# Kernel tuning notes

Hardware: AMD Instinct MI355X
Metric: run time of the kernel (lower is better)

Reference implementation:

```python
import jax, jax.numpy as jnp
import numpy as np

N_NODES = 50000
N_EDGES = 800000
D = 64  # node/edge/transformed feature size


def setup_inputs() -> dict:
    key = jax.random.key(0)
    ks = jax.random.split(key, 10)
    nodes = jax.random.normal(ks[0], (N_NODES, D), dtype=jnp.float32)
    edges = jax.random.normal(ks[1], (N_EDGES, D), dtype=jnp.float32)
    senders = jax.random.randint(ks[2], (N_EDGES,), 0, N_NODES, dtype=jnp.int32)
    receivers = jax.random.randint(ks[3], (N_EDGES,), 0, N_NODES, dtype=jnp.int32)
    # eqx.nn.Linear params: W [out, in], b [out]
    agg_edge_in = D + 2 * D       # edge + sender + receiver
    agg_node_in = D + 2 * D       # node + outgoing agg + incoming agg
    attn_in = 2 * D               # sender + receiver
    s = lambda fan_in: 1.0 / np.sqrt(fan_in)
    We = jax.random.uniform(ks[4], (D, agg_edge_in), jnp.float32, -s(agg_edge_in), s(agg_edge_in))
    be = jax.random.uniform(ks[5], (D,), jnp.float32, -s(agg_edge_in), s(agg_edge_in))
    Wn = jax.random.uniform(ks[6], (D, agg_node_in), jnp.float32, -s(agg_node_in), s(agg_node_in))
    bn = jax.random.uniform(ks[7], (D,), jnp.float32, -s(agg_node_in), s(agg_node_in))
    Wa = jax.random.uniform(ks[8], (1, attn_in), jnp.float32, -s(attn_in), s(attn_in))
    ba = jax.random.uniform(ks[9], (1,), jnp.float32, -s(attn_in), s(attn_in))
    return {"nodes": nodes, "edges": edges, "senders": senders, "receivers": receivers,
            "We": We, "be": be, "Wn": Wn, "bn": bn, "Wa": Wa, "ba": ba}


def reference(nodes, edges, senders, receivers, We, be, Wn, bn, Wa, ba):
    n = nodes.shape[0]
    sent = nodes[senders]      # [E, D] sender node features
    recv = nodes[receivers]    # [E, D] receiver node features

    # 1) update_edge_fn: concat + Linear + ReLU
    agg_e = jnp.concatenate((edges, sent, recv), axis=-1)          # [E, 3D]
    new_edges = jax.nn.relu(jnp.einsum('ei,oi->eo', agg_e, We) + be)

    # 2) attention_logit_fn: Linear on concat(sender, receiver)
    logits = jnp.einsum('ei,oi->eo', jnp.concatenate((sent, recv), axis=-1), Wa) + ba  # [E, 1]

    # 3) jraph segment_softmax over receivers (normalize per receiving node)
    seg_max = jax.ops.segment_max(logits, receivers, num_segments=n)
    ex = jnp.exp(logits - seg_max[receivers])
    denom = jax.ops.segment_sum(ex, receivers, num_segments=n)
    att = ex / denom[receivers]                                    # [E, 1]

    # attention_reduce_fn: elementwise weighting
    w_edges = new_edges * att                                      # [E, D]

    # aggregate edges for nodes (jraph default: segment_sum)
    out_agg = jax.ops.segment_sum(w_edges, senders, num_segments=n)    # outgoing
    in_agg = jax.ops.segment_sum(w_edges, receivers, num_segments=n)   # incoming

    # 4) update_node_fn: concat + Linear + ReLU
    agg_n = jnp.concatenate((nodes, out_agg, in_agg), axis=-1)     # [N, 3D]
    new_nodes = jax.nn.relu(jnp.einsum('ni,oi->no', agg_n, Wn) + bn)
    return new_nodes, w_edges
```

## Files before the change

### kernel.cpp

```cpp
#include <hip/hip_runtime.h>

#define D 64

typedef __attribute__((ext_vector_type(8))) short bf16x8;
typedef __attribute__((ext_vector_type(4))) float f32x4;

static __device__ __forceinline__ unsigned short f2bf(float x) {
    union { float f; unsigned int u; } v; v.f = x;
    const unsigned int r = (v.u + 0x7fffu + ((v.u >> 16) & 1u)) >> 16;
    return (unsigned short)r;
}
static __device__ __forceinline__ float bf2f(unsigned short u) {
    union { unsigned int i; float f; } v; v.i = ((unsigned int)u) << 16; return v.f;
}

__global__ __launch_bounds__(256)
void premix_kernel(const float* __restrict__ nodes, const float* __restrict__ We,
                   const float* __restrict__ Wa,
                   unsigned short* __restrict__ PSb, unsigned short* __restrict__ PRb,
                   float* __restrict__ ps, float* __restrict__ pr, int N)
{
    __shared__ float sWS[64][68];
    __shared__ float sWR[64][68];
    __shared__ float sX[64][68];
    __shared__ float sWa[128];

    const int t = threadIdx.x;
    const int o = t & 63;
    const int k0 = (t >> 6) * 16;
#pragma unroll
    for (int k = 0; k < 16; ++k) {
        sWS[k0 + k][o] = We[(size_t)o * 192 + 64 + k0 + k];
        sWR[k0 + k][o] = We[(size_t)o * 192 + 128 + k0 + k];
    }
    if (t < 128) sWa[t] = Wa[t];

    const int nb = blockIdx.x * 64;
    const int ln = t & 63;
    const int gn = min(nb + ln, N - 1);
    {
        const float* src = nodes + (size_t)gn * D + k0;
        const f32x4 x0 = *(const f32x4*)(src + 0);
        const f32x4 x1 = *(const f32x4*)(src + 4);
        const f32x4 x2 = *(const f32x4*)(src + 8);
        const f32x4 x3 = *(const f32x4*)(src + 12);
        sX[k0 + 0][ln] = x0.x;  sX[k0 + 1][ln] = x0.y;
        sX[k0 + 2][ln] = x0.z;  sX[k0 + 3][ln] = x0.w;
        sX[k0 + 4][ln] = x1.x;  sX[k0 + 5][ln] = x1.y;
        sX[k0 + 6][ln] = x1.z;  sX[k0 + 7][ln] = x1.w;
        sX[k0 + 8][ln] = x2.x;  sX[k0 + 9][ln] = x2.y;
        sX[k0 + 10][ln] = x2.z; sX[k0 + 11][ln] = x2.w;
        sX[k0 + 12][ln] = x3.x; sX[k0 + 13][ln] = x3.y;
        sX[k0 + 14][ln] = x3.z; sX[k0 + 15][ln] = x3.w;
    }
    __syncthreads();

    const int o0 = (t & 15) * 4;
    const int rc = (t >> 4) * 4;
    float as[4][4] = {{0.f,0.f,0.f,0.f},{0.f,0.f,0.f,0.f},{0.f,0.f,0.f,0.f},{0.f,0.f,0.f,0.f}};
    float ar[4][4] = {{0.f,0.f,0.f,0.f},{0.f,0.f,0.f,0.f},{0.f,0.f,0.f,0.f},{0.f,0.f,0.f,0.f}};

#pragma unroll 8
    for (int ci = 0; ci < 64; ++ci) {
        const f32x4 xv = *(const f32x4*)&sX[ci][rc];
        const f32x4 ws = *(const f32x4*)&sWS[ci][o0];
        const f32x4 wr = *(const f32x4*)&sWR[ci][o0];
        as[0][0] += xv.x * ws.x; as[0][1] += xv.x * ws.y; as[0][2] += xv.x * ws.z; as[0][3] += xv.x * ws.w;
        as[1][0] += xv.y * ws.x; as[1][1] += xv.y * ws.y; as[1][2] += xv.y * ws.z; as[1][3] += xv.y * ws.w;
        as[2][0] += xv.z * ws.x; as[2][1] += xv.z * ws.y; as[2][2] += xv.z * ws.z; as[2][3] += xv.z * ws.w;
        as[3][0] += xv.w * ws.x; as[3][1] += xv.w * ws.y; as[3][2] += xv.w * ws.z; as[3][3] += xv.w * ws.w;
        ar[0][0] += xv.x * wr.x; ar[0][1] += xv.x * wr.y; ar[0][2] += xv.x * wr.z; ar[0][3] += xv.x * wr.w;
        ar[1][0] += xv.y * wr.x; ar[1][1] += xv.y * wr.y; ar[1][2] += xv.y * wr.z; ar[1][3] += xv.y * wr.w;
        ar[2][0] += xv.z * wr.x; ar[2][1] += xv.z * wr.y; ar[2][2] += xv.z * wr.z; ar[2][3] += xv.z * wr.w;
        ar[3][0] += xv.w * wr.x; ar[3][1] += xv.w * wr.y; ar[3][2] += xv.w * wr.z; ar[3][3] += xv.w * wr.w;
    }

#pragma unroll
    for (int j = 0; j < 4; ++j) {
        const int n = nb + rc + j;
        if (n < N) {
            ushort4 vs, vr;
            vs.x = f2bf(as[j][0]); vs.y = f2bf(as[j][1]); vs.z = f2bf(as[j][2]); vs.w = f2bf(as[j][3]);
            vr.x = f2bf(ar[j][0]); vr.y = f2bf(ar[j][1]); vr.z = f2bf(ar[j][2]); vr.w = f2bf(ar[j][3]);
            *(ushort4*)&PSb[(size_t)n * D + o0] = vs;
            *(ushort4*)&PRb[(size_t)n * D + o0] = vr;
        }
    }

    if (t < 64 && nb + t < N) {
        float p1 = 0.f, p2 = 0.f;
#pragma unroll 8
        for (int k = 0; k < 64; ++k) {
            const float x = sX[k][t];
            p1 += x * sWa[k];
            p2 += x * sWa[64 + k];
        }
        ps[nb + t] = p1;
        pr[nb + t] = p2;
    }
}

__global__ __launch_bounds__(256)
void edge_logit_kernel(const int* __restrict__ snd, const int* __restrict__ rcv,
                       const float* __restrict__ ps, const float* __restrict__ pr,
                       const float* __restrict__ ba, float* __restrict__ elog,
                       float* __restrict__ denom, int* __restrict__ deg_out,
                       int* __restrict__ deg_in, int E)
{
    const float bav = ba[0];
    const int stride = gridDim.x * blockDim.x;
    for (int e = blockIdx.x * blockDim.x + threadIdx.x; e < E; e += stride) {
        const int s = snd[e], r = rcv[e];
        const float ex = __expf(ps[s] + pr[r] + bav);
        elog[e] = ex;
        atomicAdd(&denom[r], ex);
        atomicAdd(&deg_out[s], 1);
        atomicAdd(&deg_in[r], 1);
    }
}

__global__ __launch_bounds__(1024)
void scan_kernel(const int* __restrict__ deg_out, int* __restrict__ off_out,
                 const int* __restrict__ deg_in, int* __restrict__ off_in, int N)
{
    const int* deg = (blockIdx.x == 0) ? deg_out : deg_in;
    int* off       = (blockIdx.x == 0) ? off_out : off_in;
    __shared__ int part[1024];
    const int t = threadIdx.x;
    const int CH = (((N + 1023) / 1024) + 3) & ~3;
    const int c0 = t * CH;
    int s = 0;
    if (c0 + CH <= N) {
#pragma unroll 4
        for (int k = 0; k < CH; k += 4) {
            const int4 v = *(const int4*)&deg[c0 + k];
            s += v.x + v.y + v.z + v.w;
        }
    } else {
        for (int k = 0; k < CH; ++k) {
            const int i = c0 + k;
            if (i < N) s += deg[i];
        }
    }
    part[t] = s;
    __syncthreads();
    for (int d = 1; d < 1024; d <<= 1) {
        int v = 0;
        if (t >= d) v = part[t - d];
        __syncthreads();
        part[t] += v;
        __syncthreads();
    }
    int run = (t == 0) ? 0 : part[t - 1];
    if (c0 + CH <= N) {
#pragma unroll 4
        for (int k = 0; k < CH; k += 4) {
            const int4 v = *(const int4*)&deg[c0 + k];
            int4 w;
            w.x = run; w.y = run + v.x; w.z = w.y + v.y; w.w = w.z + v.z;
            *(int4*)&off[c0 + k] = w;
            run = w.w + v.w;
        }
    } else {
        for (int k = 0; k < CH; ++k) {
            const int i = c0 + k;
            if (i < N) { off[i] = run; run += deg[i]; }
        }
    }
    if (t == 1023) off[N] = part[1023];
}

__global__ __launch_bounds__(256)
void edge_mix_kernel(const float* __restrict__ edges, const int* __restrict__ snd,
                     const int* __restrict__ rcv, const float* __restrict__ We,
                     const float* __restrict__ be,
                     const unsigned short* __restrict__ PSb,
                     const unsigned short* __restrict__ PRb,
                     const float* __restrict__ elog, const float* __restrict__ denom,
                     const int* __restrict__ off_out, const int* __restrict__ off_in,
                     int* __restrict__ cur_out, int* __restrict__ cur_in,
                     int* __restrict__ idx_out, int* __restrict__ idx_in,
                     float* __restrict__ w_out, int E)
{
    __shared__ unsigned short sX[64][72];
    __shared__ unsigned short sW[64][72];

    const int t = threadIdx.x;
    const int eb = blockIdx.x * 64;

    if (t < 128) {
        const int e = eb + (t & 63);
        if (e < E) {
            if (t < 64) {
                const int s = snd[e];
                const int po = atomicAdd(&cur_out[s], 1);
                idx_out[off_out[s] + po] = e;
            } else {
                const int r = rcv[e];
                const int pi = atomicAdd(&cur_in[r], 1);
                idx_in[off_in[r] + pi] = e;
            }
        }
    }

    {
        const int le = t & 63;
        const int k0 = (t >> 6) * 16;
        const int ge = min(eb + le, E - 1);
        const float* xsrc = edges + (size_t)ge * D + k0;
        const float* wsrc = We + (size_t)le * 192 + k0;
        const f32x4 x0 = *(const f32x4*)(xsrc + 0);
        const f32x4 x1 = *(const f32x4*)(xsrc + 4);
        const f32x4 x2 = *(const f32x4*)(xsrc + 8);
        const f32x4 x3 = *(const f32x4*)(xsrc + 12);
        const f32x4 w0 = *(const f32x4*)(wsrc + 0);
        const f32x4 w1 = *(const f32x4*)(wsrc + 4);
        const f32x4 w2 = *(const f32x4*)(wsrc + 8);
        const f32x4 w3 = *(const f32x4*)(wsrc + 12);
        uint4 xp, wp;
        xp.x = (unsigned)f2bf(x0.x) | ((unsigned)f2bf(x0.y) << 16);
        xp.y = (unsigned)f2bf(x0.z) | ((unsigned)f2bf(x0.w) << 16);
        xp.z = (unsigned)f2bf(x1.x) | ((unsigned)f2bf(x1.y) << 16);
        xp.w = (unsigned)f2bf(x1.z) | ((unsigned)f2bf(x1.w) << 16);
        *(uint4*)&sX[le][k0] = xp;
        xp.x = (unsigned)f2bf(x2.x) | ((unsigned)f2bf(x2.y) << 16);
        xp.y = (unsigned)f2bf(x2.z) | ((unsigned)f2bf(x2.w) << 16);
        xp.z = (unsigned)f2bf(x3.x) | ((unsigned)f2bf(x3.y) << 16);
        xp.w = (unsigned)f2bf(x3.z) | ((unsigned)f2bf(x3.w) << 16);
        *(uint4*)&sX[le][k0 + 8] = xp;
        wp.x = (unsigned)f2bf(w0.x) | ((unsigned)f2bf(w0.y) << 16);
        wp.y = (unsigned)f2bf(w0.z) | ((unsigned)f2bf(w0.w) << 16);
        wp.z = (unsigned)f2bf(w1.x) | ((unsigned)f2bf(w1.y) << 16);
        wp.w = (unsigned)f2bf(w1.z) | ((unsigned)f2bf(w1.w) << 16);
        *(uint4*)&sW[le][k0] = wp;
        wp.x = (unsigned)f2bf(w2.x) | ((unsigned)f2bf(w2.y) << 16);
        wp.y = (unsigned)f2bf(w2.z) | ((unsigned)f2bf(w2.w) << 16);
        wp.z = (unsigned)f2bf(w3.x) | ((unsigned)f2bf(w3.y) << 16);
        wp.w = (unsigned)f2bf(w3.z) | ((unsigned)f2bf(w3.w) << 16);
        *(uint4*)&sW[le][k0 + 8] = wp;
    }
    __syncthreads();

    const int w   = t >> 6;
    const int l   = t & 63;
    const int r16 = l & 15;
    const int kb  = l >> 4;

    f32x4 acc[4] = {{0.f,0.f,0.f,0.f},{0.f,0.f,0.f,0.f},{0.f,0.f,0.f,0.f},{0.f,0.f,0.f,0.f}};
    const int er = w * 16 + r16;

#pragma unroll
    for (int kt = 0; kt < 2; ++kt) {
        const int kof = kt * 32 + kb * 8;
        const bf16x8 x = *(const bf16x8*)&sX[er][kof];
#pragma unroll
        for (int n = 0; n < 4; ++n) {
            const bf16x8 wv = *(const bf16x8*)&sW[n * 16 + r16][kof];
            acc[n] = __builtin_amdgcn_mfma_f32_16x16x32_bf16(wv, x, acc[n], 0, 0, 0);
        }
    }

    const int e = eb + er;
    if (e < E) {
        const int s = snd[e];
        const int r = rcv[e];
        const float att = elog[e] / denom[r];
        const int o0 = kb * 4;
        const unsigned short* psr = PSb + (size_t)s * D + o0;
        const unsigned short* prr = PRb + (size_t)r * D + o0;
        float* wo = w_out + (size_t)e * D + o0;
#pragma unroll
        for (int n = 0; n < 4; ++n) {
            const ushort4 psv = *(const ushort4*)(psr + n * 16);
            const ushort4 prv = *(const ushort4*)(prr + n * 16);
            const f32x4 bev = *(const f32x4*)&be[n * 16 + o0];
            f32x4 wv;
            wv.x = fmaxf(acc[n][0] + bf2f(psv.x) + bf2f(prv.x) + bev.x, 0.f) * att;
            wv.y = fmaxf(acc[n][1] + bf2f(psv.y) + bf2f(prv.y) + bev.y, 0.f) * att;
            wv.z = fmaxf(acc[n][2] + bf2f(psv.z) + bf2f(prv.z) + bev.z, 0.f) * att;
            wv.w = fmaxf(acc[n][3] + bf2f(psv.w) + bf2f(prv.w) + bev.w, 0.f) * att;
            *(f32x4*)(wo + n * 16) = wv;
        }
    }
}

__global__ __launch_bounds__(256)
void agg_kernel(const float* __restrict__ w_edges,
                const int* __restrict__ idx_out, const int* __restrict__ off_out,
                const int* __restrict__ idx_in, const int* __restrict__ off_in,
                float* __restrict__ out_agg, float* __restrict__ in_agg, int N)
{
    const int lane = threadIdx.x & 63;
    const int wid  = (blockIdx.x * blockDim.x + threadIdx.x) >> 6;
    if (wid >= 2 * N) return;
    const bool is_out = wid < N;
    const int node = is_out ? wid : wid - N;
    const int* __restrict__ idx = is_out ? idx_out : idx_in;
    const int* __restrict__ off = is_out ? off_out : off_in;
    float* __restrict__ dst = is_out ? out_agg : in_agg;

    const int a = off[node], b = off[node + 1];
    float acc = 0.f;
    int j = a;
    for (; j + 3 < b; j += 4) {
        const int e0 = idx[j], e1 = idx[j + 1], e2 = idx[j + 2], e3 = idx[j + 3];
        const float v0 = w_edges[(size_t)e0 * D + lane];
        const float v1 = w_edges[(size_t)e1 * D + lane];
        const float v2 = w_edges[(size_t)e2 * D + lane];
        const float v3 = w_edges[(size_t)e3 * D + lane];
        acc += v0 + v1 + v2 + v3;
    }
    for (; j < b; ++j) acc += w_edges[(size_t)idx[j] * D + lane];
    dst[(size_t)node * D + lane] = acc;
}

__global__ __launch_bounds__(256)
void node_out_kernel(const float* __restrict__ nodes, const float* __restrict__ oag,
                     const float* __restrict__ iag, const float* __restrict__ Wn,
                     const float* __restrict__ bn, float* __restrict__ out, int N)
{
    __shared__ float sW[64][68];
    __shared__ float sX[64][68];

    const int t = threadIdx.x;
    const int o = t & 63;
    const int k0 = (t >> 6) * 16;
    const int nb = blockIdx.x * 64;
    const int ln = t & 63;
    const int gn = min(nb + ln, N - 1);
    const int o0 = (t & 15) * 4;
    const int rc = (t >> 4) * 4;

    float acc[4][4] = {{0.f,0.f,0.f,0.f},{0.f,0.f,0.f,0.f},{0.f,0.f,0.f,0.f},{0.f,0.f,0.f,0.f}};

#pragma unroll
    for (int g = 0; g < 3; ++g) {
        const float* xbase = (g == 0) ? nodes : ((g == 1) ? oag : iag);
        const float* src = xbase + (size_t)gn * D + k0;
        const f32x4 x0 = *(const f32x4*)(src + 0);
        const f32x4 x1 = *(const f32x4*)(src + 4);
        const f32x4 x2 = *(const f32x4*)(src + 8);
        const f32x4 x3 = *(const f32x4*)(src + 12);
        __syncthreads();
#pragma unroll
        for (int k = 0; k < 16; ++k) {
            sW[k0 + k][o] = Wn[(size_t)o * 192 + g * 64 + k0 + k];
        }
        sX[k0 + 0][ln] = x0.x;  sX[k0 + 1][ln] = x0.y;
        sX[k0 + 2][ln] = x0.z;  sX[k0 + 3][ln] = x0.w;
        sX[k0 + 4][ln] = x1.x;  sX[k0 + 5][ln] = x1.y;
        sX[k0 + 6][ln] = x1.z;  sX[k0 + 7][ln] = x1.w;
        sX[k0 + 8][ln] = x2.x;  sX[k0 + 9][ln] = x2.y;
        sX[k0 + 10][ln] = x2.z; sX[k0 + 11][ln] = x2.w;
        sX[k0 + 12][ln] = x3.x; sX[k0 + 13][ln] = x3.y;
        sX[k0 + 14][ln] = x3.z; sX[k0 + 15][ln] = x3.w;
        __syncthreads();
#pragma unroll 8
        for (int ci = 0; ci < 64; ++ci) {
            const f32x4 xv = *(const f32x4*)&sX[ci][rc];
            const f32x4 wv = *(const f32x4*)&sW[ci][o0];
            acc[0][0] += xv.x * wv.x; acc[0][1] += xv.x * wv.y; acc[0][2] += xv.x * wv.z; acc[0][3] += xv.x * wv.w;
            acc[1][0] += xv.y * wv.x; acc[1][1] += xv.y * wv.y; acc[1][2] += xv.y * wv.z; acc[1][3] += xv.y * wv.w;
            acc[2][0] += xv.z * wv.x; acc[2][1] += xv.z * wv.y; acc[2][2] += xv.z * wv.z; acc[2][3] += xv.z * wv.w;
            acc[3][0] += xv.w * wv.x; acc[3][1] += xv.w * wv.y; acc[3][2] += xv.w * wv.z; acc[3][3] += xv.w * wv.w;
        }
    }

    const f32x4 bnv = *(const f32x4*)&bn[o0];
#pragma unroll
    for (int j = 0; j < 4; ++j) {
        const int n = nb + rc + j;
        if (n < N) {
            f32x4 y;
            y.x = fmaxf(acc[j][0] + bnv.x, 0.f);
            y.y = fmaxf(acc[j][1] + bnv.y, 0.f);
            y.z = fmaxf(acc[j][2] + bnv.z, 0.f);
            y.w = fmaxf(acc[j][3] + bnv.w, 0.f);
            *(f32x4*)&out[(size_t)n * D + o0] = y;
        }
    }
}

extern "C" void kernel_launch(void* const* d_in, const int* in_sizes, int n_in,
                              void* d_out, int out_size, void* d_ws, size_t ws_size,
                              hipStream_t stream) {
    const float* nodes = (const float*)d_in[0];
    const float* edges = (const float*)d_in[1];
    const int*   snd   = (const int*)d_in[2];
    const int*   rcv   = (const int*)d_in[3];
    const float* We    = (const float*)d_in[4];
    const float* be    = (const float*)d_in[5];
    const float* Wn    = (const float*)d_in[6];
    const float* bn    = (const float*)d_in[7];
    const float* Wa    = (const float*)d_in[8];
    const float* ba    = (const float*)d_in[9];

    const int N = in_sizes[0] / D;
    const int E = in_sizes[2];

    float* out_nodes = (float*)d_out;
    float* w_out     = (float*)d_out + (size_t)N * D;

    char* w = (char*)d_ws;
    float* denom   = (float*)w;                 w += (size_t)N * 4;
    int*   deg_out = (int*)w;                   w += (size_t)N * 4;
    int*   deg_in  = (int*)w;                   w += (size_t)N * 4;
    int*   cur_out = (int*)w;                   w += (size_t)N * 4;
    int*   cur_in  = (int*)w;                   w += (size_t)N * 4;
    float* ps      = (float*)w;                 w += (size_t)N * 4;
    float* pr      = (float*)w;                 w += (size_t)N * 4;
    int*   off_out = (int*)w;                   w += (size_t)(N + 1) * 4;
    int*   off_in  = (int*)w;                   w += (size_t)(N + 1) * 4;
    float* elog    = (float*)w;                 w += (size_t)E * 4;
    int*   idx_out = (int*)w;                   w += (size_t)E * 4;
    int*   idx_in  = (int*)w;                   w += (size_t)E * 4;
    unsigned short* PSb = (unsigned short*)w;   w += (size_t)N * D * 2;
    unsigned short* PRb = (unsigned short*)w;   w += (size_t)N * D * 2;
    float* out_agg = (float*)w;                 w += (size_t)N * D * 4;
    float* in_agg  = (float*)w;

    hipMemsetAsync(denom, 0, (size_t)5 * N * 4, stream);

    premix_kernel<<<(N + 63) / 64, 256, 0, stream>>>(nodes, We, Wa, PSb, PRb, ps, pr, N);

    edge_logit_kernel<<<1024, 256, 0, stream>>>(snd, rcv, ps, pr, ba, elog,
                                                denom, deg_out, deg_in, E);

    scan_kernel<<<2, 1024, 0, stream>>>(deg_out, off_out, deg_in, off_in, N);

    edge_mix_kernel<<<(E + 63) / 64, 256, 0, stream>>>(edges, snd, rcv, We, be,
                                                       PSb, PRb, elog, denom,
                                                       off_out, off_in, cur_out, cur_in,
                                                       idx_out, idx_in, w_out, E);

    agg_kernel<<<(2 * N + 3) / 4, 256, 0, stream>>>(w_out, idx_out, off_out,
                                                    idx_in, off_in, out_agg, in_agg, N);

    node_out_kernel<<<(N + 63) / 64, 256, 0, stream>>>(nodes, out_agg, in_agg,
                                                       Wn, bn, out_nodes, N);
}
```

Baseline: 503.1 us.

## Make edge_mix persistent with register-resident weights and direct MFMA operand loads

```diff
diff --git a/kernel.cpp b/kernel.cpp
--- a/kernel.cpp
+++ b/kernel.cpp
@@ -12,6 +12,14 @@
 }
 static __device__ __forceinline__ float bf2f(unsigned short u) {
     union { unsigned int i; float f; } v; v.i = ((unsigned int)u) << 16; return v.f;
+}
+static __device__ __forceinline__ bf16x8 pack8(const f32x4 a, const f32x4 b) {
+    union { bf16x8 v; unsigned int u[4]; } p;
+    p.u[0] = (unsigned)f2bf(a.x) | ((unsigned)f2bf(a.y) << 16);
+    p.u[1] = (unsigned)f2bf(a.z) | ((unsigned)f2bf(a.w) << 16);
+    p.u[2] = (unsigned)f2bf(b.x) | ((unsigned)f2bf(b.y) << 16);
+    p.u[3] = (unsigned)f2bf(b.z) | ((unsigned)f2bf(b.w) << 16);
+    return p.v;
 }
 
 __global__ __launch_bounds__(256)
@@ -182,104 +190,71 @@
                      int* __restrict__ idx_out, int* __restrict__ idx_in,
                      float* __restrict__ w_out, int E)
 {
-    __shared__ unsigned short sX[64][72];
-    __shared__ unsigned short sW[64][72];
-
-    const int t = threadIdx.x;
-    const int eb = blockIdx.x * 64;
-
-    if (t < 128) {
-        const int e = eb + (t & 63);
-        if (e < E) {
-            if (t < 64) {
-                const int s = snd[e];
-                const int po = atomicAdd(&cur_out[s], 1);
-                idx_out[off_out[s] + po] = e;
-            } else {
-                const int r = rcv[e];
-                const int pi = atomicAdd(&cur_in[r], 1);
-                idx_in[off_in[r] + pi] = e;
-            }
-        }
-    }
-
-    {
-        const int le = t & 63;
-        const int k0 = (t >> 6) * 16;
-        const int ge = min(eb + le, E - 1);
-        const float* xsrc = edges + (size_t)ge * D + k0;
-        const float* wsrc = We + (size_t)le * 192 + k0;
-        const f32x4 x0 = *(const f32x4*)(xsrc + 0);
-        const f32x4 x1 = *(const f32x4*)(xsrc + 4);
-        const f32x4 x2 = *(const f32x4*)(xsrc + 8);
-        const f32x4 x3 = *(const f32x4*)(xsrc + 12);
-        const f32x4 w0 = *(const f32x4*)(wsrc + 0);
-        const f32x4 w1 = *(const f32x4*)(wsrc + 4);
-        const f32x4 w2 = *(const f32x4*)(wsrc + 8);
-        const f32x4 w3 = *(const f32x4*)(wsrc + 12);
-        uint4 xp, wp;
-        xp.x = (unsigned)f2bf(x0.x) | ((unsigned)f2bf(x0.y) << 16);
-        xp.y = (unsigned)f2bf(x0.z) | ((unsigned)f2bf(x0.w) << 16);
-        xp.z = (unsigned)f2bf(x1.x) | ((unsigned)f2bf(x1.y) << 16);
-        xp.w = (unsigned)f2bf(x1.z) | ((unsigned)f2bf(x1.w) << 16);
-        *(uint4*)&sX[le][k0] = xp;
-        xp.x = (unsigned)f2bf(x2.x) | ((unsigned)f2bf(x2.y) << 16);
-        xp.y = (unsigned)f2bf(x2.z) | ((unsigned)f2bf(x2.w) << 16);
-        xp.z = (unsigned)f2bf(x3.x) | ((unsigned)f2bf(x3.y) << 16);
-        xp.w = (unsigned)f2bf(x3.z) | ((unsigned)f2bf(x3.w) << 16);
-        *(uint4*)&sX[le][k0 + 8] = xp;
-        wp.x = (unsigned)f2bf(w0.x) | ((unsigned)f2bf(w0.y) << 16);
-        wp.y = (unsigned)f2bf(w0.z) | ((unsigned)f2bf(w0.w) << 16);
-        wp.z = (unsigned)f2bf(w1.x) | ((unsigned)f2bf(w1.y) << 16);
-        wp.w = (unsigned)f2bf(w1.z) | ((unsigned)f2bf(w1.w) << 16);
-        *(uint4*)&sW[le][k0] = wp;
-        wp.x = (unsigned)f2bf(w2.x) | ((unsigned)f2bf(w2.y) << 16);
-        wp.y = (unsigned)f2bf(w2.z) | ((unsigned)f2bf(w2.w) << 16);
-        wp.z = (unsigned)f2bf(w3.x) | ((unsigned)f2bf(w3.y) << 16);
-        wp.w = (unsigned)f2bf(w3.z) | ((unsigned)f2bf(w3.w) << 16);
-        *(uint4*)&sW[le][k0 + 8] = wp;
-    }
-    __syncthreads();
-
+    const int t   = threadIdx.x;
     const int w   = t >> 6;
     const int l   = t & 63;
     const int r16 = l & 15;
     const int kb  = l >> 4;
 
-    f32x4 acc[4] = {{0.f,0.f,0.f,0.f},{0.f,0.f,0.f,0.f},{0.f,0.f,0.f,0.f},{0.f,0.f,0.f,0.f}};
-    const int er = w * 16 + r16;
-
-#pragma unroll
-    for (int kt = 0; kt < 2; ++kt) {
-        const int kof = kt * 32 + kb * 8;
-        const bf16x8 x = *(const bf16x8*)&sX[er][kof];
-#pragma unroll
-        for (int n = 0; n < 4; ++n) {
-            const bf16x8 wv = *(const bf16x8*)&sW[n * 16 + r16][kof];
-            acc[n] = __builtin_amdgcn_mfma_f32_16x16x32_bf16(wv, x, acc[n], 0, 0, 0);
-        }
-    }
-
-    const int e = eb + er;
-    if (e < E) {
-        const int s = snd[e];
-        const int r = rcv[e];
-        const float att = elog[e] / denom[r];
-        const int o0 = kb * 4;
-        const unsigned short* psr = PSb + (size_t)s * D + o0;
-        const unsigned short* prr = PRb + (size_t)r * D + o0;
-        float* wo = w_out + (size_t)e * D + o0;
-#pragma unroll
-        for (int n = 0; n < 4; ++n) {
-            const ushort4 psv = *(const ushort4*)(psr + n * 16);
-            const ushort4 prv = *(const ushort4*)(prr + n * 16);
-            const f32x4 bev = *(const f32x4*)&be[n * 16 + o0];
-            f32x4 wv;
-            wv.x = fmaxf(acc[n][0] + bf2f(psv.x) + bf2f(prv.x) + bev.x, 0.f) * att;
-            wv.y = fmaxf(acc[n][1] + bf2f(psv.y) + bf2f(prv.y) + bev.y, 0.f) * att;
-            wv.z = fmaxf(acc[n][2] + bf2f(psv.z) + bf2f(prv.z) + bev.z, 0.f) * att;
-            wv.w = fmaxf(acc[n][3] + bf2f(psv.w) + bf2f(prv.w) + bev.w, 0.f) * att;
-            *(f32x4*)(wo + n * 16) = wv;
+    bf16x8 aw[4][2];
+#pragma unroll
+    for (int n = 0; n < 4; ++n) {
+#pragma unroll
+        for (int kt = 0; kt < 2; ++kt) {
+            const float* src = We + (size_t)(n * 16 + r16) * 192 + kt * 32 + kb * 8;
+            aw[n][kt] = pack8(*(const f32x4*)(src), *(const f32x4*)(src + 4));
+        }
+    }
+    f32x4 bev[4];
+#pragma unroll
+    for (int n = 0; n < 4; ++n) bev[n] = *(const f32x4*)&be[n * 16 + kb * 4];
+
+    const int nt = (E + 63) >> 6;
+    for (int tile = blockIdx.x; tile < nt; tile += gridDim.x) {
+        const int e  = tile * 64 + w * 16 + r16;
+        const int ec = min(e, E - 1);
+        const int s  = snd[ec];
+        const int r  = rcv[ec];
+
+        bf16x8 bx[2];
+#pragma unroll
+        for (int kt = 0; kt < 2; ++kt) {
+            const float* src = edges + (size_t)ec * D + kt * 32 + kb * 8;
+            bx[kt] = pack8(*(const f32x4*)(src), *(const f32x4*)(src + 4));
+        }
+
+        f32x4 acc[4] = {{0.f,0.f,0.f,0.f},{0.f,0.f,0.f,0.f},{0.f,0.f,0.f,0.f},{0.f,0.f,0.f,0.f}};
+#pragma unroll
+        for (int kt = 0; kt < 2; ++kt) {
+#pragma unroll
+            for (int n = 0; n < 4; ++n)
+                acc[n] = __builtin_amdgcn_mfma_f32_16x16x32_bf16(aw[n][kt], bx[kt], acc[n], 0, 0, 0);
+        }
+
+        if (e < E) {
+            if (kb == 0) {
+                const int po = atomicAdd(&cur_out[s], 1);
+                idx_out[off_out[s] + po] = e;
+            } else if (kb == 1) {
+                const int pi = atomicAdd(&cur_in[r], 1);
+                idx_in[off_in[r] + pi] = e;
+            }
+            const float att = elog[e] / denom[r];
+            const int o0 = kb * 4;
+            const unsigned short* psr = PSb + (size_t)s * D + o0;
+            const unsigned short* prr = PRb + (size_t)r * D + o0;
+            float* wo = w_out + (size_t)e * D + o0;
+#pragma unroll
+            for (int n = 0; n < 4; ++n) {
+                const ushort4 psv = *(const ushort4*)(psr + n * 16);
+                const ushort4 prv = *(const ushort4*)(prr + n * 16);
+                f32x4 wv;
+                wv.x = fmaxf(acc[n][0] + bf2f(psv.x) + bf2f(prv.x) + bev[n].x, 0.f) * att;
+                wv.y = fmaxf(acc[n][1] + bf2f(psv.y) + bf2f(prv.y) + bev[n].y, 0.f) * att;
+                wv.z = fmaxf(acc[n][2] + bf2f(psv.z) + bf2f(prv.z) + bev[n].z, 0.f) * att;
+                wv.w = fmaxf(acc[n][3] + bf2f(psv.w) + bf2f(prv.w) + bev[n].w, 0.f) * att;
+                *(f32x4*)(wo + n * 16) = wv;
+            }
         }
     }
 }
@@ -428,10 +403,12 @@
 
     scan_kernel<<<2, 1024, 0, stream>>>(deg_out, off_out, deg_in, off_in, N);
 
-    edge_mix_kernel<<<(E + 63) / 64, 256, 0, stream>>>(edges, snd, rcv, We, be,
-                                                       PSb, PRb, elog, denom,
-                                                       off_out, off_in, cur_out, cur_in,
-                                                       idx_out, idx_in, w_out, E);
+    const int nt = (E + 63) / 64;
+    const int eblocks = nt < 2048 ? nt : 2048;
+    edge_mix_kernel<<<eblocks, 256, 0, stream>>>(edges, snd, rcv, We, be,
+                                                 PSb, PRb, elog, denom,
+                                                 off_out, off_in, cur_out, cur_in,
+                                                 idx_out, idx_in, w_out, E);
 
     agg_kernel<<<(2 * N + 3) / 4, 256, 0, stream>>>(w_out, idx_out, off_out,
                                                     idx_in, off_in, out_agg, in_agg, N);
```

Result: faster. 483.3 us (-3.9%).
